# Kernel optimization log

Hardware: AMD Instinct MI355X
Metric: run time of the kernel (lower is better)

## Reference

```python
import jax, jax.numpy as jnp
import numpy as np
from jax import lax


def _dw(x, w):
    # x: (C,H,W), w: (C,1,kh,kw) -> depthwise 'same' conv, groups=C
    return lax.conv_general_dilated(
        x[None], w, window_strides=(1, 1), padding='SAME',
        dimension_numbers=('NCHW', 'OIHW', 'NCHW'),
        feature_group_count=x.shape[0])[0]

_dw_b = jax.vmap(_dw)  # per-batch-element dynamic depthwise conv


def setup_inputs() -> dict:
    key = jax.random.key(0)
    ks = jax.random.split(key, 6)
    Q, B, C, H, W = 100, 8, 64, 256, 256
    return {
        'query': jax.random.normal(ks[0], (Q, B, C), jnp.float32),
        'value': jax.random.normal(ks[1], (B, C, H, W), jnp.float32),
        'hard_sigmoid_masks': jnp.zeros((1,), jnp.float32),
        'pos2': jnp.zeros((1,), jnp.float32),
        'pos3': jnp.zeros((1,), jnp.float32),
        'Wl': jax.random.normal(ks[2], (18, 100), jnp.float32) * 0.1,
        'bl': jax.random.normal(ks[3], (18,), jnp.float32) * 0.1,
        'Wd': jax.random.normal(ks[4], (100, 18), jnp.float32) * 0.1,
        'bd': jax.random.normal(ks[5], (100,), jnp.float32) * 0.1,
    }


def reference(query, value, hard_sigmoid_masks, pos2, pos3, Wl, bl, Wd, bd):
    Qn, B, C = query.shape
    # weight_linear on query.permute(1,2,0): (B,C,100) @ Wl.T + bl -> (B,C,18)
    conv1d = jnp.einsum('qbc,kq->bck', query, Wl) + bl
    former = conv1d[..., :9].reshape(B, C, 1, 3, 3)   # filt1
    wk = conv1d[..., 9:].reshape(B, C, 1, 3, 3)        # weight_conv1d

    y_temp = _dw_b(value, former)                       # (B,C,H,W)
    diff = jnp.exp(-(value - y_temp) ** 2)
    filt2 = lax.stop_gradient(jnp.abs(wk))
    y_diff9 = _dw_b(diff, filt2)
    vd = value * diff
    res = _dw_b(vd, wk)
    weights_d = wk.sum(axis=(2, 3), keepdims=True)      # (B,C,1,1,3) -> 1x3 kernel
    res_diff = _dw_b(vd, weights_d)
    y_diff = (res - res_diff) / (y_diff9 + 1e-10)
    y = y_temp - y_diff

    weight1 = jnp.concatenate([former.reshape(B, C, 9), wk.reshape(B, C, 9)], axis=-1)
    q = jnp.einsum('bck,nk->bcn', weight1, Wd) + bd     # (B,C,100)
    return (q.transpose(2, 0, 1), y)
```

## Files before the change

### kernel.cpp

```cpp
#include <hip/hip_runtime.h>
#include <math.h>

#define HH 256
#define WW 256
#define BC 512
#define QN 100

__global__ __launch_bounds__(128) void prep_kernel(
    const float* __restrict__ query,
    const float* __restrict__ Wl,
    const float* __restrict__ bl,
    const float* __restrict__ Wd,
    const float* __restrict__ bd,
    float* __restrict__ qout,
    float* __restrict__ coef)
{
    const int bc = blockIdx.x;
    const int t  = threadIdx.x;
    __shared__ float qcol[QN];
    __shared__ float c18[18];

    if (t < QN) qcol[t] = query[t * BC + bc];
    __syncthreads();

    if (t < 18) {
        float acc = bl[t];
        const float* wrow = Wl + t * QN;
        #pragma unroll 4
        for (int qi = 0; qi < QN; ++qi) acc += qcol[qi] * wrow[qi];
        c18[t] = acc;
    }
    __syncthreads();

    if (t < QN) {
        float acc = bd[t];
        const float* wrow = Wd + t * 18;
        #pragma unroll
        for (int k = 0; k < 18; ++k) acc += c18[k] * wrow[k];
        qout[t * BC + bc] = acc;
    }

    if (t < 18) {
        coef[bc * 32 + t] = c18[t];
    } else if (t < 27) {
        coef[bc * 32 + t] = fabsf(c18[t - 9]);
    } else if (t < 30) {
        int j = t - 27;
        coef[bc * 32 + t] = c18[9 + j] + c18[12 + j] + c18[15 + j];
    }
}

__global__ __launch_bounds__(256) void fused_kernel(
    const float* __restrict__ value,
    const float* __restrict__ coef,
    float* __restrict__ yout)
{
    const int bc  = blockIdx.z;
    const int h0  = blockIdx.y * 64;
    const int w0  = blockIdx.x * 64;
    const int tid = threadIdx.x;
    const int wave = tid >> 6;
    const int lane = tid & 63;

    __shared__ __align__(16) float sval[68][68];
    __shared__ __align__(16) float sdiff[66][68];

    const float* cp = coef + bc * 32;
    float fco[9], wk[9], awk[9], ws[3];
    #pragma unroll
    for (int i = 0; i < 9; ++i) { fco[i] = cp[i]; wk[i] = cp[9 + i]; awk[i] = cp[18 + i]; }
    ws[0] = cp[27]; ws[1] = cp[28]; ws[2] = cp[29];

    const float* vp = value + (size_t)bc * (HH * WW);

    #pragma unroll
    for (int it = 0; it < 10; ++it) {
        int idx = tid + it * 256;
        if (idx < 68 * 34) {
            int r = idx / 34;
            int m = idx - r * 34;
            int h = h0 - 2 + r;
            int w = w0 - 2 + 2 * m;
            float2 v = make_float2(0.f, 0.f);
            if ((unsigned)h < HH) {
                const float* rowp = vp + h * WW;
                if ((unsigned)w < WW)       v.x = rowp[w];
                if ((unsigned)(w + 1) < WW) v.y = rowp[w + 1];
            }
            *(float2*)&sval[r][2 * m] = v;
        }
    }
    __syncthreads();

    {
        const int lo = (wave < 2) ? 17 * wave : 34 + 16 * (wave - 2);
        const int hi = (wave < 2) ? lo + 17 : lo + 16;
        const int x  = lane;
        float t00 = sval[lo][x],     t01 = sval[lo][x + 1],     t02 = sval[lo][x + 2];
        float t10 = sval[lo + 1][x], t11 = sval[lo + 1][x + 1], t12 = sval[lo + 1][x + 2];
        for (int r = lo; r < hi; ++r) {
            float t20 = sval[r + 2][x], t21 = sval[r + 2][x + 1], t22 = sval[r + 2][x + 2];
            float yt = fco[0]*t00 + fco[1]*t01 + fco[2]*t02
                     + fco[3]*t10 + fco[4]*t11 + fco[5]*t12
                     + fco[6]*t20 + fco[7]*t21 + fco[8]*t22;
            float e = t11 - yt;
            float d = __expf(-e * e);
            if ((unsigned)(h0 - 1 + r) >= HH || (unsigned)(w0 - 1 + x) >= WW) d = 0.f;
            sdiff[r][x] = d;
            t00 = t10; t01 = t11; t02 = t12;
            t10 = t20; t11 = t21; t12 = t22;
        }
    }

    if (tid < 132) {
        int r = tid >> 1;
        int c = 64 + (tid & 1);
        float yt = 0.f;
        #pragma unroll
        for (int u = 0; u < 3; ++u)
            #pragma unroll
            for (int v = 0; v < 3; ++v)
                yt += fco[u * 3 + v] * sval[r + u][c + v];
        float e = sval[r + 1][c + 1] - yt;
        float d = __expf(-e * e);
        if ((unsigned)(h0 - 1 + r) >= HH || (unsigned)(w0 - 1 + c) >= WW) d = 0.f;
        sdiff[r][c] = d;
    }
    __syncthreads();

    {
        const int y0 = wave * 16;
        const int x  = lane;
        float* dst = yout + (size_t)bc * (HH * WW) + (size_t)(h0 + y0) * WW + (w0 + x);

        float sd0[3], sd1[3], sd2[3];
        float sv0[3], sv1[3], sv2[3];
        float vd0[3], vd1[3], vd2[3];
        #pragma unroll
        for (int b = 0; b < 3; ++b) {
            sd0[b] = sdiff[y0][x + b];
            sv0[b] = sval[y0 + 1][x + 1 + b];
            vd0[b] = sd0[b] * sv0[b];
            sd1[b] = sdiff[y0 + 1][x + b];
            sv1[b] = sval[y0 + 2][x + 1 + b];
            vd1[b] = sd1[b] * sv1[b];
        }
        #pragma unroll
        for (int i = 0; i < 16; ++i) {
            const int y = y0 + i;
            #pragma unroll
            for (int b = 0; b < 3; ++b) {
                sd2[b] = sdiff[y + 2][x + b];
                sv2[b] = sval[y + 3][x + 1 + b];
                vd2[b] = sd2[b] * sv2[b];
            }
            float yt  = fco[0]*sv0[0] + fco[1]*sv0[1] + fco[2]*sv0[2]
                      + fco[3]*sv1[0] + fco[4]*sv1[1] + fco[5]*sv1[2]
                      + fco[6]*sv2[0] + fco[7]*sv2[1] + fco[8]*sv2[2];
            float yd9 = 1e-10f
                      + awk[0]*sd0[0] + awk[1]*sd0[1] + awk[2]*sd0[2]
                      + awk[3]*sd1[0] + awk[4]*sd1[1] + awk[5]*sd1[2]
                      + awk[6]*sd2[0] + awk[7]*sd2[1] + awk[8]*sd2[2];
            float rs  = wk[0]*vd0[0] + wk[1]*vd0[1] + wk[2]*vd0[2]
                      + wk[3]*vd1[0] + wk[4]*vd1[1] + wk[5]*vd1[2]
                      + wk[6]*vd2[0] + wk[7]*vd2[1] + wk[8]*vd2[2];
            float rd  = ws[0]*vd1[0] + ws[1]*vd1[1] + ws[2]*vd1[2];
            float inv = __builtin_amdgcn_rcpf(yd9);
            dst[i * WW] = yt - (rs - rd) * inv;
            #pragma unroll
            for (int b = 0; b < 3; ++b) {
                sd0[b] = sd1[b]; sv0[b] = sv1[b]; vd0[b] = vd1[b];
                sd1[b] = sd2[b]; sv1[b] = sv2[b]; vd1[b] = vd2[b];
            }
        }
    }
}

extern "C" void kernel_launch(void* const* d_in, const int* in_sizes, int n_in,
                              void* d_out, int out_size, void* d_ws, size_t ws_size,
                              hipStream_t stream) {
    const float* query = (const float*)d_in[0];
    const float* value = (const float*)d_in[1];
    const float* Wl    = (const float*)d_in[5];
    const float* bl    = (const float*)d_in[6];
    const float* Wd    = (const float*)d_in[7];
    const float* bd    = (const float*)d_in[8];

    float* out   = (float*)d_out;
    float* qout  = out;
    float* yout  = out + QN * BC;
    float* coef  = (float*)d_ws;

    prep_kernel<<<BC, 128, 0, stream>>>(query, Wl, bl, Wd, bd, qout, coef);

    dim3 grid(WW / 64, HH / 64, BC);
    fused_kernel<<<grid, 256, 0, stream>>>(value, coef, yout);
}
```

Before: 307.6 us.

## Compute 4x4 outputs per thread with float4 LDS access and simplified numerator

Both stencil phases are restructured so each thread handles four adjacent columns over four rows, loading shared-memory rows as float4 and writing results with float4 stores. The numerator res - res_diff is folded algebraically: the middle-row taps cancel against the summed 1x3 kernel, leaving six taps on row differences. Boundary masks become multiplications instead of branches, and launch bounds request four blocks per CU. This aims to cut LDS instruction count and redundant neighbour loads, but raises register pressure per thread and may change bank-conflict behaviour.

```diff
diff --git a/kernel.cpp b/kernel.cpp
--- a/kernel.cpp
+++ b/kernel.cpp
@@ -50,7 +50,7 @@
     }
 }
 
-__global__ __launch_bounds__(256) void fused_kernel(
+__global__ __launch_bounds__(256, 4) void fused_kernel(
     const float* __restrict__ value,
     const float* __restrict__ coef,
     float* __restrict__ yout)
@@ -61,15 +61,16 @@
     const int tid = threadIdx.x;
     const int wave = tid >> 6;
     const int lane = tid & 63;
+    const int grp  = lane >> 4;
+    const int x4   = (lane & 15) << 2;
 
     __shared__ __align__(16) float sval[68][68];
     __shared__ __align__(16) float sdiff[66][68];
 
     const float* cp = coef + bc * 32;
-    float fco[9], wk[9], awk[9], ws[3];
+    float fco[9], wk[9], awk[9];
     #pragma unroll
     for (int i = 0; i < 9; ++i) { fco[i] = cp[i]; wk[i] = cp[9 + i]; awk[i] = cp[18 + i]; }
-    ws[0] = cp[27]; ws[1] = cp[28]; ws[2] = cp[29];
 
     const float* vp = value + (size_t)bc * (HH * WW);
 
@@ -93,85 +94,146 @@
     __syncthreads();
 
     {
-        const int lo = (wave < 2) ? 17 * wave : 34 + 16 * (wave - 2);
-        const int hi = (wave < 2) ? lo + 17 : lo + 16;
-        const int x  = lane;
-        float t00 = sval[lo][x],     t01 = sval[lo][x + 1],     t02 = sval[lo][x + 2];
-        float t10 = sval[lo + 1][x], t11 = sval[lo + 1][x + 1], t12 = sval[lo + 1][x + 2];
-        for (int r = lo; r < hi; ++r) {
-            float t20 = sval[r + 2][x], t21 = sval[r + 2][x + 1], t22 = sval[r + 2][x + 2];
-            float yt = fco[0]*t00 + fco[1]*t01 + fco[2]*t02
-                     + fco[3]*t10 + fco[4]*t11 + fco[5]*t12
-                     + fco[6]*t20 + fco[7]*t21 + fco[8]*t22;
-            float e = t11 - yt;
-            float d = __expf(-e * e);
-            if ((unsigned)(h0 - 1 + r) >= HH || (unsigned)(w0 - 1 + x) >= WW) d = 0.f;
-            sdiff[r][x] = d;
-            t00 = t10; t01 = t11; t02 = t12;
-            t10 = t20; t11 = t21; t12 = t22;
-        }
-    }
-
-    if (tid < 132) {
-        int r = tid >> 1;
-        int c = 64 + (tid & 1);
-        float yt = 0.f;
-        #pragma unroll
-        for (int u = 0; u < 3; ++u)
-            #pragma unroll
-            for (int v = 0; v < 3; ++v)
-                yt += fco[u * 3 + v] * sval[r + u][c + v];
-        float e = sval[r + 1][c + 1] - yt;
-        float d = __expf(-e * e);
-        if ((unsigned)(h0 - 1 + r) >= HH || (unsigned)(w0 - 1 + c) >= WW) d = 0.f;
-        sdiff[r][c] = d;
+        const int r0 = (wave * 4 + grp) * 4;
+        float cm[4];
+        #pragma unroll
+        for (int co = 0; co < 4; ++co)
+            cm[co] = ((unsigned)(w0 - 1 + x4 + co) < WW) ? 1.f : 0.f;
+
+        float a0[8], a1[8], a2[8];
+        *(float4*)&a0[0] = *(const float4*)&sval[r0][x4];
+        *(float4*)&a0[4] = *(const float4*)&sval[r0][x4 + 4];
+        *(float4*)&a1[0] = *(const float4*)&sval[r0 + 1][x4];
+        *(float4*)&a1[4] = *(const float4*)&sval[r0 + 1][x4 + 4];
+        #pragma unroll
+        for (int i = 0; i < 4; ++i) {
+            const int r = r0 + i;
+            *(float4*)&a2[0] = *(const float4*)&sval[r + 2][x4];
+            *(float4*)&a2[4] = *(const float4*)&sval[r + 2][x4 + 4];
+            const float rm = ((unsigned)(h0 - 1 + r) < HH) ? 1.f : 0.f;
+            float4 od;
+            #pragma unroll
+            for (int co = 0; co < 4; ++co) {
+                float yt = fco[0]*a0[co] + fco[1]*a0[co+1] + fco[2]*a0[co+2]
+                         + fco[3]*a1[co] + fco[4]*a1[co+1] + fco[5]*a1[co+2]
+                         + fco[6]*a2[co] + fco[7]*a2[co+1] + fco[8]*a2[co+2];
+                float e = a1[co + 1] - yt;
+                (&od.x)[co] = __expf(-e * e) * (rm * cm[co]);
+            }
+            *(float4*)&sdiff[r][x4] = od;
+            #pragma unroll
+            for (int j = 0; j < 8; ++j) { a0[j] = a1[j]; a1[j] = a2[j]; }
+        }
+    }
+
+    if (tid < 66) {
+        const int r = tid;
+        float a0[4], a1[4], a2[4];
+        *(float4*)a0 = *(const float4*)&sval[r][64];
+        *(float4*)a1 = *(const float4*)&sval[r + 1][64];
+        *(float4*)a2 = *(const float4*)&sval[r + 2][64];
+        const float rm  = ((unsigned)(h0 - 1 + r) < HH) ? 1.f : 0.f;
+        const float c65 = (w0 + 64 < WW) ? 1.f : 0.f;
+        float2 od;
+        {
+            float yt = fco[0]*a0[0] + fco[1]*a0[1] + fco[2]*a0[2]
+                     + fco[3]*a1[0] + fco[4]*a1[1] + fco[5]*a1[2]
+                     + fco[6]*a2[0] + fco[7]*a2[1] + fco[8]*a2[2];
+            float e = a1[1] - yt;
+            od.x = __expf(-e * e) * rm;
+        }
+        {
+            float yt = fco[0]*a0[1] + fco[1]*a0[2] + fco[2]*a0[3]
+                     + fco[3]*a1[1] + fco[4]*a1[2] + fco[5]*a1[3]
+                     + fco[6]*a2[1] + fco[7]*a2[2] + fco[8]*a2[3];
+            float e = a1[2] - yt;
+            od.y = __expf(-e * e) * (rm * c65);
+        }
+        *(float2*)&sdiff[r][64] = od;
+    }
+
+    if ((unsigned)(tid - 128) < 32u) {
+        const int u  = tid - 128;
+        const int r  = 64 + (u >> 4);
+        const int c0 = (u & 15) << 2;
+        float a0[8], a1[8], a2[8];
+        *(float4*)&a0[0] = *(const float4*)&sval[r][c0];
+        *(float4*)&a0[4] = *(const float4*)&sval[r][c0 + 4];
+        *(float4*)&a1[0] = *(const float4*)&sval[r + 1][c0];
+        *(float4*)&a1[4] = *(const float4*)&sval[r + 1][c0 + 4];
+        *(float4*)&a2[0] = *(const float4*)&sval[r + 2][c0];
+        *(float4*)&a2[4] = *(const float4*)&sval[r + 2][c0 + 4];
+        const float rm = ((unsigned)(h0 - 1 + r) < HH) ? 1.f : 0.f;
+        float4 od;
+        #pragma unroll
+        for (int co = 0; co < 4; ++co) {
+            const float cmv = ((unsigned)(w0 - 1 + c0 + co) < WW) ? 1.f : 0.f;
+            float yt = fco[0]*a0[co] + fco[1]*a0[co+1] + fco[2]*a0[co+2]
+                     + fco[3]*a1[co] + fco[4]*a1[co+1] + fco[5]*a1[co+2]
+                     + fco[6]*a2[co] + fco[7]*a2[co+1] + fco[8]*a2[co+2];
+            float e = a1[co + 1] - yt;
+            (&od.x)[co] = __expf(-e * e) * (rm * cmv);
+        }
+        *(float4*)&sdiff[r][c0] = od;
     }
     __syncthreads();
 
     {
-        const int y0 = wave * 16;
-        const int x  = lane;
-        float* dst = yout + (size_t)bc * (HH * WW) + (size_t)(h0 + y0) * WW + (w0 + x);
-
-        float sd0[3], sd1[3], sd2[3];
-        float sv0[3], sv1[3], sv2[3];
-        float vd0[3], vd1[3], vd2[3];
-        #pragma unroll
-        for (int b = 0; b < 3; ++b) {
-            sd0[b] = sdiff[y0][x + b];
-            sv0[b] = sval[y0 + 1][x + 1 + b];
-            vd0[b] = sd0[b] * sv0[b];
-            sd1[b] = sdiff[y0 + 1][x + b];
-            sv1[b] = sval[y0 + 2][x + 1 + b];
-            vd1[b] = sd1[b] * sv1[b];
-        }
-        #pragma unroll
-        for (int i = 0; i < 16; ++i) {
+        const int y0 = (wave * 4 + grp) * 4;
+        float* dst = yout + (size_t)bc * (HH * WW) + (size_t)(h0 + y0) * WW + (w0 + x4);
+
+        float sd0[8], sd1[8], sd2[8];
+        float sv0[8], sv1[8], sv2[8];
+        float vd0[6], vd1[6], vd2[6];
+        *(float4*)&sd0[0] = *(const float4*)&sdiff[y0][x4];
+        *(float4*)&sd0[4] = *(const float4*)&sdiff[y0][x4 + 4];
+        *(float4*)&sd1[0] = *(const float4*)&sdiff[y0 + 1][x4];
+        *(float4*)&sd1[4] = *(const float4*)&sdiff[y0 + 1][x4 + 4];
+        *(float4*)&sv0[0] = *(const float4*)&sval[y0 + 1][x4];
+        *(float4*)&sv0[4] = *(const float4*)&sval[y0 + 1][x4 + 4];
+        *(float4*)&sv1[0] = *(const float4*)&sval[y0 + 2][x4];
+        *(float4*)&sv1[4] = *(const float4*)&sval[y0 + 2][x4 + 4];
+        #pragma unroll
+        for (int j = 0; j < 6; ++j) {
+            vd0[j] = sd0[j] * sv0[j + 1];
+            vd1[j] = sd1[j] * sv1[j + 1];
+        }
+        #pragma unroll
+        for (int i = 0; i < 4; ++i) {
             const int y = y0 + i;
-            #pragma unroll
-            for (int b = 0; b < 3; ++b) {
-                sd2[b] = sdiff[y + 2][x + b];
-                sv2[b] = sval[y + 3][x + 1 + b];
-                vd2[b] = sd2[b] * sv2[b];
-            }
-            float yt  = fco[0]*sv0[0] + fco[1]*sv0[1] + fco[2]*sv0[2]
-                      + fco[3]*sv1[0] + fco[4]*sv1[1] + fco[5]*sv1[2]
-                      + fco[6]*sv2[0] + fco[7]*sv2[1] + fco[8]*sv2[2];
-            float yd9 = 1e-10f
-                      + awk[0]*sd0[0] + awk[1]*sd0[1] + awk[2]*sd0[2]
-                      + awk[3]*sd1[0] + awk[4]*sd1[1] + awk[5]*sd1[2]
-                      + awk[6]*sd2[0] + awk[7]*sd2[1] + awk[8]*sd2[2];
-            float rs  = wk[0]*vd0[0] + wk[1]*vd0[1] + wk[2]*vd0[2]
-                      + wk[3]*vd1[0] + wk[4]*vd1[1] + wk[5]*vd1[2]
-                      + wk[6]*vd2[0] + wk[7]*vd2[1] + wk[8]*vd2[2];
-            float rd  = ws[0]*vd1[0] + ws[1]*vd1[1] + ws[2]*vd1[2];
-            float inv = __builtin_amdgcn_rcpf(yd9);
-            dst[i * WW] = yt - (rs - rd) * inv;
-            #pragma unroll
-            for (int b = 0; b < 3; ++b) {
-                sd0[b] = sd1[b]; sv0[b] = sv1[b]; vd0[b] = vd1[b];
-                sd1[b] = sd2[b]; sv1[b] = sv2[b]; vd1[b] = vd2[b];
-            }
+            *(float4*)&sd2[0] = *(const float4*)&sdiff[y + 2][x4];
+            *(float4*)&sd2[4] = *(const float4*)&sdiff[y + 2][x4 + 4];
+            *(float4*)&sv2[0] = *(const float4*)&sval[y + 3][x4];
+            *(float4*)&sv2[4] = *(const float4*)&sval[y + 3][x4 + 4];
+            float dv0[6], dv2[6];
+            #pragma unroll
+            for (int j = 0; j < 6; ++j) {
+                vd2[j] = sd2[j] * sv2[j + 1];
+                dv0[j] = vd0[j] - vd1[j];
+                dv2[j] = vd2[j] - vd1[j];
+            }
+            float4 o;
+            #pragma unroll
+            for (int co = 0; co < 4; ++co) {
+                float yt  = fco[0]*sv0[co+1] + fco[1]*sv0[co+2] + fco[2]*sv0[co+3]
+                          + fco[3]*sv1[co+1] + fco[4]*sv1[co+2] + fco[5]*sv1[co+3]
+                          + fco[6]*sv2[co+1] + fco[7]*sv2[co+2] + fco[8]*sv2[co+3];
+                float yd9 = 1e-10f
+                          + awk[0]*sd0[co] + awk[1]*sd0[co+1] + awk[2]*sd0[co+2]
+                          + awk[3]*sd1[co] + awk[4]*sd1[co+1] + awk[5]*sd1[co+2]
+                          + awk[6]*sd2[co] + awk[7]*sd2[co+1] + awk[8]*sd2[co+2];
+                float num = wk[0]*dv0[co] + wk[1]*dv0[co+1] + wk[2]*dv0[co+2]
+                          + wk[6]*dv2[co] + wk[7]*dv2[co+1] + wk[8]*dv2[co+2];
+                (&o.x)[co] = yt - num * __builtin_amdgcn_rcpf(yd9);
+            }
+            *(float4*)&dst[i * WW] = o;
+            #pragma unroll
+            for (int j = 0; j < 8; ++j) {
+                sd0[j] = sd1[j]; sd1[j] = sd2[j];
+                sv0[j] = sv1[j]; sv1[j] = sv2[j];
+            }
+            #pragma unroll
+            for (int j = 0; j < 6; ++j) { vd0[j] = vd1[j]; vd1[j] = vd2[j]; }
         }
     }
 }
```

Result: no change. 306.3 us (-0.4%).

## Replace LDS tiling with register row-streaming and wave shuffles for halos

Applied to the files above, without the earlier changes.

The fused kernel no longer stages 64x64 tiles plus halos in shared memory. Each wave now owns a full-width 32-row band, loads float4 per lane, gets horizontal neighbours through lane shuffles, and keeps a rolling 4-row register window of values and diff rows, writing results with float4 stores. This removes LDS traffic, the block barriers and most of the halo re-reads, and it algebraically drops the centre row of the weighted sums by folding res-res_diff into six taps. In exchange each thread holds more live registers, and the grid becomes 2x512 blocks with a serial 32-row loop per wave.

```diff
diff --git a/kernel.cpp b/kernel.cpp
--- a/kernel.cpp
+++ b/kernel.cpp
@@ -5,6 +5,7 @@
 #define WW 256
 #define BC 512
 #define QN 100
+#define RBAND 32
 
 __global__ __launch_bounds__(128) void prep_kernel(
     const float* __restrict__ query,
@@ -50,128 +51,113 @@
     }
 }
 
-__global__ __launch_bounds__(256) void fused_kernel(
+__global__ __launch_bounds__(256, 4) void fused_kernel(
     const float* __restrict__ value,
     const float* __restrict__ coef,
     float* __restrict__ yout)
 {
-    const int bc  = blockIdx.z;
-    const int h0  = blockIdx.y * 64;
-    const int w0  = blockIdx.x * 64;
-    const int tid = threadIdx.x;
-    const int wave = tid >> 6;
-    const int lane = tid & 63;
+    const int bc   = blockIdx.z;
+    const int wave = threadIdx.x >> 6;
+    const int lane = threadIdx.x & 63;
+    const int band = blockIdx.x * 4 + wave;
+    const int r0   = band * RBAND;
+    const int x4   = lane << 2;
 
-    __shared__ __align__(16) float sval[68][68];
-    __shared__ __align__(16) float sdiff[66][68];
+    const bool l0  = (lane == 0);
+    const bool l63 = (lane == 63);
 
     const float* cp = coef + bc * 32;
-    float fco[9], wk[9], awk[9], ws[3];
+    float fco[9], awk[9], wk6[6];
     #pragma unroll
-    for (int i = 0; i < 9; ++i) { fco[i] = cp[i]; wk[i] = cp[9 + i]; awk[i] = cp[18 + i]; }
-    ws[0] = cp[27]; ws[1] = cp[28]; ws[2] = cp[29];
+    for (int i = 0; i < 9; ++i) { fco[i] = cp[i]; awk[i] = cp[18 + i]; }
+    wk6[0] = cp[9];  wk6[1] = cp[10]; wk6[2] = cp[11];
+    wk6[3] = cp[15]; wk6[4] = cp[16]; wk6[5] = cp[17];
 
-    const float* vp = value + (size_t)bc * (HH * WW);
+    const float* vbase = value + (size_t)bc * (HH * WW);
+    float*       obase = yout  + (size_t)bc * (HH * WW);
 
-    #pragma unroll
-    for (int it = 0; it < 10; ++it) {
-        int idx = tid + it * 256;
-        if (idx < 68 * 34) {
-            int r = idx / 34;
-            int m = idx - r * 34;
-            int h = h0 - 2 + r;
-            int w = w0 - 2 + 2 * m;
-            float2 v = make_float2(0.f, 0.f);
-            if ((unsigned)h < HH) {
-                const float* rowp = vp + h * WW;
-                if ((unsigned)w < WW)       v.x = rowp[w];
-                if ((unsigned)(w + 1) < WW) v.y = rowp[w + 1];
+    float v[4][6];
+    float d[4][6];
+
+    auto LOADV = [&](int r, float* row) {
+        if ((unsigned)r < HH) {
+            const float4 q = *(const float4*)(vbase + r * WW + x4);
+            row[1] = q.x; row[2] = q.y; row[3] = q.z; row[4] = q.w;
+            float left  = __shfl_up(q.w, 1);
+            float right = __shfl_down(q.x, 1);
+            row[0] = l0  ? 0.f : left;
+            row[5] = l63 ? 0.f : right;
+        } else {
+            #pragma unroll
+            for (int m = 0; m < 6; ++m) row[m] = 0.f;
+        }
+    };
+
+    auto COMPD = [&](int r, const float* va, const float* vb, const float* vc,
+                     float* drow) {
+        if ((unsigned)r < HH) {
+            float d4[4];
+            #pragma unroll
+            for (int c = 0; c < 4; ++c) {
+                float yt = fco[0]*va[c] + fco[1]*va[c+1] + fco[2]*va[c+2]
+                         + fco[3]*vb[c] + fco[4]*vb[c+1] + fco[5]*vb[c+2]
+                         + fco[6]*vc[c] + fco[7]*vc[c+1] + fco[8]*vc[c+2];
+                float e = vb[c + 1] - yt;
+                d4[c] = __expf(-e * e);
             }
-            *(float2*)&sval[r][2 * m] = v;
+            drow[1] = d4[0]; drow[2] = d4[1]; drow[3] = d4[2]; drow[4] = d4[3];
+            float left  = __shfl_up(d4[3], 1);
+            float right = __shfl_down(d4[0], 1);
+            drow[0] = l0  ? 0.f : left;
+            drow[5] = l63 ? 0.f : right;
+        } else {
+            #pragma unroll
+            for (int m = 0; m < 6; ++m) drow[m] = 0.f;
         }
-    }
-    __syncthreads();
+    };
 
-    {
-        const int lo = (wave < 2) ? 17 * wave : 34 + 16 * (wave - 2);
-        const int hi = (wave < 2) ? lo + 17 : lo + 16;
-        const int x  = lane;
-        float t00 = sval[lo][x],     t01 = sval[lo][x + 1],     t02 = sval[lo][x + 2];
-        float t10 = sval[lo + 1][x], t11 = sval[lo + 1][x + 1], t12 = sval[lo + 1][x + 2];
-        for (int r = lo; r < hi; ++r) {
-            float t20 = sval[r + 2][x], t21 = sval[r + 2][x + 1], t22 = sval[r + 2][x + 2];
-            float yt = fco[0]*t00 + fco[1]*t01 + fco[2]*t02
-                     + fco[3]*t10 + fco[4]*t11 + fco[5]*t12
-                     + fco[6]*t20 + fco[7]*t21 + fco[8]*t22;
-            float e = t11 - yt;
-            float d = __expf(-e * e);
-            if ((unsigned)(h0 - 1 + r) >= HH || (unsigned)(w0 - 1 + x) >= WW) d = 0.f;
-            sdiff[r][x] = d;
-            t00 = t10; t01 = t11; t02 = t12;
-            t10 = t20; t11 = t21; t12 = t22;
+    auto OUTROW = [&](int h, const float* vp, const float* vq, const float* vs,
+                      const float* dp, const float* dq, const float* ds) {
+        float dv0[6], dv2[6];
+        #pragma unroll
+        for (int m = 0; m < 6; ++m) {
+            float mid = dq[m] * vq[m];
+            dv0[m] = dp[m] * vp[m] - mid;
+            dv2[m] = ds[m] * vs[m] - mid;
         }
-    }
+        float4 o;
+        #pragma unroll
+        for (int c = 0; c < 4; ++c) {
+            float yt  = fco[0]*vp[c] + fco[1]*vp[c+1] + fco[2]*vp[c+2]
+                      + fco[3]*vq[c] + fco[4]*vq[c+1] + fco[5]*vq[c+2]
+                      + fco[6]*vs[c] + fco[7]*vs[c+1] + fco[8]*vs[c+2];
+            float yd9 = 1e-10f
+                      + awk[0]*dp[c] + awk[1]*dp[c+1] + awk[2]*dp[c+2]
+                      + awk[3]*dq[c] + awk[4]*dq[c+1] + awk[5]*dq[c+2]
+                      + awk[6]*ds[c] + awk[7]*ds[c+1] + awk[8]*ds[c+2];
+            float num = wk6[0]*dv0[c] + wk6[1]*dv0[c+1] + wk6[2]*dv0[c+2]
+                      + wk6[3]*dv2[c] + wk6[4]*dv2[c+1] + wk6[5]*dv2[c+2];
+            (&o.x)[c] = yt - num * __builtin_amdgcn_rcpf(yd9);
+        }
+        *(float4*)(obase + h * WW + x4) = o;
+    };
 
-    if (tid < 132) {
-        int r = tid >> 1;
-        int c = 64 + (tid & 1);
-        float yt = 0.f;
+    LOADV(r0 - 2, v[0]);
+    LOADV(r0 - 1, v[1]);
+    LOADV(r0,     v[2]);
+    LOADV(r0 + 1, v[3]);
+    COMPD(r0 - 1, v[0], v[1], v[2], d[0]);
+    COMPD(r0,     v[1], v[2], v[3], d[1]);
+
+    for (int io = 0; io < RBAND; io += 4) {
         #pragma unroll
-        for (int u = 0; u < 3; ++u)
-            #pragma unroll
-            for (int v = 0; v < 3; ++v)
-                yt += fco[u * 3 + v] * sval[r + u][c + v];
-        float e = sval[r + 1][c + 1] - yt;
-        float d = __expf(-e * e);
-        if ((unsigned)(h0 - 1 + r) >= HH || (unsigned)(w0 - 1 + c) >= WW) d = 0.f;
-        sdiff[r][c] = d;
-    }
-    __syncthreads();
-
-    {
-        const int y0 = wave * 16;
-        const int x  = lane;
-        float* dst = yout + (size_t)bc * (HH * WW) + (size_t)(h0 + y0) * WW + (w0 + x);
-
-        float sd0[3], sd1[3], sd2[3];
-        float sv0[3], sv1[3], sv2[3];
-        float vd0[3], vd1[3], vd2[3];
-        #pragma unroll
-        for (int b = 0; b < 3; ++b) {
-            sd0[b] = sdiff[y0][x + b];
-            sv0[b] = sval[y0 + 1][x + 1 + b];
-            vd0[b] = sd0[b] * sv0[b];
-            sd1[b] = sdiff[y0 + 1][x + b];
-            sv1[b] = sval[y0 + 2][x + 1 + b];
-            vd1[b] = sd1[b] * sv1[b];
-        }
-        #pragma unroll
-        for (int i = 0; i < 16; ++i) {
-            const int y = y0 + i;
-            #pragma unroll
-            for (int b = 0; b < 3; ++b) {
-                sd2[b] = sdiff[y + 2][x + b];
-                sv2[b] = sval[y + 3][x + 1 + b];
-                vd2[b] = sd2[b] * sv2[b];
-            }
-            float yt  = fco[0]*sv0[0] + fco[1]*sv0[1] + fco[2]*sv0[2]
-                      + fco[3]*sv1[0] + fco[4]*sv1[1] + fco[5]*sv1[2]
-                      + fco[6]*sv2[0] + fco[7]*sv2[1] + fco[8]*sv2[2];
-            float yd9 = 1e-10f
-                      + awk[0]*sd0[0] + awk[1]*sd0[1] + awk[2]*sd0[2]
-                      + awk[3]*sd1[0] + awk[4]*sd1[1] + awk[5]*sd1[2]
-                      + awk[6]*sd2[0] + awk[7]*sd2[1] + awk[8]*sd2[2];
-            float rs  = wk[0]*vd0[0] + wk[1]*vd0[1] + wk[2]*vd0[2]
-                      + wk[3]*vd1[0] + wk[4]*vd1[1] + wk[5]*vd1[2]
-                      + wk[6]*vd2[0] + wk[7]*vd2[1] + wk[8]*vd2[2];
-            float rd  = ws[0]*vd1[0] + ws[1]*vd1[1] + ws[2]*vd1[2];
-            float inv = __builtin_amdgcn_rcpf(yd9);
-            dst[i * WW] = yt - (rs - rd) * inv;
-            #pragma unroll
-            for (int b = 0; b < 3; ++b) {
-                sd0[b] = sd1[b]; sv0[b] = sv1[b]; vd0[b] = vd1[b];
-                sd1[b] = sd2[b]; sv1[b] = sv2[b]; vd1[b] = vd2[b];
-            }
+        for (int j = 0; j < 4; ++j) {
+            const int h = r0 + io + j;
+            LOADV(h + 2, v[j & 3]);
+            COMPD(h + 1, v[(j + 2) & 3], v[(j + 3) & 3], v[j & 3],
+                  d[(j + 2) & 3]);
+            OUTROW(h, v[(j + 1) & 3], v[(j + 2) & 3], v[(j + 3) & 3],
+                   d[j & 3], d[(j + 1) & 3], d[(j + 2) & 3]);
         }
     }
 }
@@ -193,6 +179,6 @@
 
     prep_kernel<<<BC, 128, 0, stream>>>(query, Wl, bl, Wd, bd, qout, coef);
 
-    dim3 grid(WW / 64, HH / 64, BC);
+    dim3 grid(HH / (RBAND * 4), 1, BC);
     fused_kernel<<<grid, 256, 0, stream>>>(value, coef, yout);
 }
```

Result: faster. 279.2 us (-9.2%).
